# Kernel tuning notes

Hardware: AMD Instinct MI355X
Metric: run time of the kernel (lower is better)

The kernel has to match this reference:

```python
import jax, jax.numpy as jnp
import numpy as np

RADIUS = 0.1
NSAMPLE = 32
NUM_KP = 15
KP_EXTENT = 1.0
DENSITY_PARAM = 5.0
EXTENT = 2.0 * KP_EXTENT * RADIUS / DENSITY_PARAM  # 0.04
K_RADIUS = 1.5 * EXTENT                            # 0.06
C_IN, C_OUT = 64, 128
BN_EPS = 1e-5


def make_kernel_points():
    # Deterministic stand-in for create_kernel_points: first point at center
    # ('center' fixed mode), remaining points quasi-uniform in a ball of K_RADIUS.
    rs = np.random.RandomState(0)
    d = rs.randn(NUM_KP - 1, 3)
    d /= np.linalg.norm(d, axis=1, keepdims=True) + 1e-9
    r = rs.rand(NUM_KP - 1, 1) ** (1.0 / 3.0)
    pts = np.concatenate([np.zeros((1, 3)), d * r * K_RADIUS], axis=0)
    return jnp.asarray(pts, dtype=jnp.float32)  # [K, 3]


def ball_group(query_xyz, support_xyz, support_mask, radius, nsample):
    """Masked ordered ball query. Returns idx [B,N1,S] int32 and mask [B,N1,S] float."""
    # [B, N1, N2] squared distances (dominant memory traffic)
    d2 = jnp.sum((query_xyz[:, :, None, :] - support_xyz[:, None, :, :]) ** 2, axis=-1)
    valid = (d2 < radius * radius) & (support_mask[:, None, :] > 0)
    order = jnp.cumsum(valid.astype(jnp.int32), axis=-1) - 1  # rank among valid, per row
    in_cap = valid & (order < nsample)
    slot = jnp.where(in_cap, order, nsample)  # overflow -> dump slot
    B, N1, N2 = d2.shape
    j = jnp.broadcast_to(jnp.arange(N2, dtype=jnp.int32), (B, N1, N2))
    b = jnp.arange(B)[:, None, None]
    n = jnp.arange(N1)[None, :, None]
    idx = jnp.zeros((B, N1, nsample + 1), jnp.int32).at[b, n, slot].set(j)[..., :nsample]
    cnt = jnp.sum(in_cap.astype(jnp.int32), axis=-1)  # [B, N1]
    nb_mask = jnp.arange(nsample)[None, None, :] < cnt[:, :, None]
    idx = jnp.where(nb_mask, idx, idx[:, :, :1])  # pad with first neighbor
    return idx, nb_mask.astype(jnp.float32)


def setup_inputs() -> dict:
    key = jax.random.key(0)
    ks = jax.random.split(key, 6)
    B, N1, N2 = 4, 2048, 8192
    query_xyz = jax.random.uniform(ks[0], (B, N1, 3), dtype=jnp.float32)
    support_xyz = jax.random.uniform(ks[1], (B, N2, 3), dtype=jnp.float32)
    query_mask = jnp.ones((B, N1), jnp.float32)
    support_mask = jnp.ones((B, N2), jnp.float32)
    support_features = jax.random.normal(ks[2], (B, C_IN, N2), dtype=jnp.float32)
    kernel_weights = jax.random.normal(ks[3], (NUM_KP, C_IN), dtype=jnp.float32) * (1.0 / np.sqrt(C_IN))
    W_out = jax.random.normal(ks[4], (C_OUT, C_IN), dtype=jnp.float32) * (1.0 / np.sqrt(C_IN))
    gamma = jnp.ones((C_OUT,), jnp.float32)
    beta = jnp.zeros((C_OUT,), jnp.float32)
    return {
        "query_xyz": query_xyz, "support_xyz": support_xyz,
        "query_mask": query_mask, "support_mask": support_mask,
        "support_features": support_features, "K_points": make_kernel_points(),
        "kernel_weights": kernel_weights, "W_out": W_out,
        "gamma": gamma, "beta": beta,
    }


def reference(query_xyz, support_xyz, query_mask, support_mask, support_features,
              K_points, kernel_weights, W_out, gamma, beta):
    idx, nb_mask = ball_group(query_xyz, support_xyz, support_mask, RADIUS, NSAMPLE)
    # gather neighbor features: [B, N2, C] -> [B, N1, S, C]
    feats_t = jnp.transpose(support_features, (0, 2, 1))
    nbr_feats = jnp.take_along_axis(feats_t[:, None, :, :],
                                    idx[:, :, :, None], axis=2)  # [B,N1,S,C]
    # grouped relative positions: [B, N1, S, 3]
    grouped_xyz = jnp.take_along_axis(support_xyz[:, None, :, :],
                                      idx[:, :, :, None], axis=2)
    rel_pos = grouped_xyz - query_xyz[:, :, None, :]
    # kernel-point distances: [B, N1, S, K]
    diff = rel_pos[:, :, :, None, :] - K_points[None, None, None, :, :]
    sq_d = jnp.sum(diff * diff, axis=-1)
    # linear influence, then permute to [B, N1, K, S]
    w = jnp.clip(1.0 - jnp.sqrt(sq_d) / EXTENT, 0.0, None)
    w = jnp.transpose(w, (0, 1, 3, 2))
    feature_mask = nb_mask + (1.0 - query_mask[:, :, None])  # [B,N1,S]
    w = w * feature_mask[:, :, None, :]
    # weighted sum over neighbors: [B, N1, K, C]
    weighted = jnp.einsum('bnks,bnsc->bnkc', w, nbr_feats)
    out = jnp.sum(weighted * kernel_weights[None, None, :, :], axis=2)  # [B,N1,C]
    out = jnp.transpose(out, (0, 2, 1))  # [B, C_in, N1]
    # out_conv: 1x1 conv (no bias) + BatchNorm1d (training-mode batch stats) + ReLU
    out = jnp.einsum('oc,bcn->bon', W_out, out)  # [B, C_out, N1]
    mean = jnp.mean(out, axis=(0, 2), keepdims=True)
    var = jnp.mean((out - mean) ** 2, axis=(0, 2), keepdims=True)
    out = (out - mean) * jax.lax.rsqrt(var + BN_EPS)
    out = out * gamma[None, :, None] + beta[None, :, None]
    return jax.nn.relu(out)
```

## Files before the change

### kernel.cpp

```cpp
#include <hip/hip_runtime.h>
#include <stdint.h>
#include <limits.h>

#define BATCH 4
#define N1D   2048
#define N2D   8192
#define NSAMP 32
#define NKP   15
#define CIN   64
#define COUT  128

#define RAD2    0.01f
#define INV_EXT 25.0f
#define BN_EPS  1e-5f
#define CMARG   0.1000001f

#define NWAVE 4
#define QPB   NWAVE
#define NCELL 1000
#define MAXC  96

#define WS_PTS4   0
#define WS_BPTS   131072
#define WS_FEATT  262144
#define WS_OUT2   2367488
#define WS_CS     3416064
#define WS_CNT    3420160
#define WS_CUR    3424256

__device__ __forceinline__ int cell_of(float x, float y, float z) {
  int cx = (int)(x*10.f); cx = cx < 0 ? 0 : (cx > 9 ? 9 : cx);
  int cy = (int)(y*10.f); cy = cy < 0 ? 0 : (cy > 9 ? 9 : cy);
  int cz = (int)(z*10.f); cz = cz < 0 ? 0 : (cz > 9 ? 9 : cz);
  return (cx*10 + cy)*10 + cz;
}

__global__ __launch_bounds__(256) void pg_prep(
    const float* __restrict__ sxyz, const float* __restrict__ smask,
    const float* __restrict__ sfeat, float4* __restrict__ pts4,
    float* __restrict__ featT, int* __restrict__ cellCnt)
{
  __shared__ float tile[64*65];
  const int t  = threadIdx.x;
  const int bt = blockIdx.x;

  if (bt >= 512) {
    const int idx = bt - 512;
    const int bb  = idx >> 5;
    const int i   = ((idx & 31) << 8) + t;
    if (smask[bb*N2D + i] > 0.f) {
      const float* p = sxyz + ((size_t)bb*N2D + i)*3;
      atomicAdd(&cellCnt[bb*1024 + cell_of(p[0], p[1], p[2])], 1);
    }
    return;
  }

  const int b  = bt >> 7;
  const int j0 = (bt & 127) * 64;
  if (t < 64) {
    const int g = bt*64 + t;
    pts4[g] = make_float4(sxyz[g*3+0], sxyz[g*3+1], sxyz[g*3+2], 0.f);
  }
  const float* src = sfeat + (size_t)(b*CIN)*N2D + j0;
#pragma unroll
  for (int i = 0; i < 4; ++i) {
    const int c  = i*16 + (t >> 4);
    const int j4 = (t & 15) * 4;
    const float4 v = *(const float4*)(src + (size_t)c*N2D + j4);
    tile[c*65 + j4+0] = v.x;
    tile[c*65 + j4+1] = v.y;
    tile[c*65 + j4+2] = v.z;
    tile[c*65 + j4+3] = v.w;
  }
  __syncthreads();
  float* dstb = featT + (size_t)(b*N2D + j0) * CIN;
#pragma unroll
  for (int r = 0; r < 4; ++r) {
    const int j  = r*16 + (t >> 4);
    const int c4 = (t & 15) * 4;
    float4 v;
    v.x = tile[(c4+0)*65 + j];
    v.y = tile[(c4+1)*65 + j];
    v.z = tile[(c4+2)*65 + j];
    v.w = tile[(c4+3)*65 + j];
    *(float4*)(dstb + j*CIN + c4) = v;
  }
}

__global__ __launch_bounds__(256) void pg_scan(
    const int* __restrict__ cellCnt, int* __restrict__ cellStart,
    int* __restrict__ cellCur)
{
  __shared__ int off_s[NCELL+1];
  __shared__ int wsum[4];
  const int t    = threadIdx.x;
  const int lane = t & 63;
  const int wv   = t >> 6;
  const int bb   = blockIdx.x;
  const int* cnt = cellCnt + bb*1024;

  int c0 = 0, c1 = 0, c2 = 0, c3 = 0, v = 0;
  if (t < 250) {
    c0 = cnt[t*4+0]; c1 = cnt[t*4+1]; c2 = cnt[t*4+2]; c3 = cnt[t*4+3];
    v = c0 + c1 + c2 + c3;
  }
  int x = v;
#pragma unroll
  for (int off = 1; off < 64; off <<= 1) {
    int y = __shfl_up(x, off);
    if (lane >= off) x += y;
  }
  if (lane == 63) wsum[wv] = x;
  __syncthreads();
  int base = 0;
#pragma unroll
  for (int w = 0; w < 4; ++w) if (w < wv) base += wsum[w];
  const int excl = base + x - v;
  if (t < 250) {
    int o = excl;
    off_s[t*4+0] = o; o += c0;
    off_s[t*4+1] = o; o += c1;
    off_s[t*4+2] = o; o += c2;
    off_s[t*4+3] = o;
  }
  if (t == 0) off_s[NCELL] = wsum[0]+wsum[1]+wsum[2]+wsum[3];
  __syncthreads();
  for (int i = t; i < NCELL; i += 256) {
    const int o = off_s[i];
    cellStart[bb*(NCELL+1) + i] = o;
    cellCur[bb*1024 + i] = o;
  }
  if (t == 0) cellStart[bb*(NCELL+1) + NCELL] = off_s[NCELL];
}

__global__ __launch_bounds__(256) void pg_scatter(
    const float* __restrict__ sxyz, const float* __restrict__ smask,
    int* __restrict__ cellCur, float4* __restrict__ bpts)
{
  const int idx = blockIdx.x;
  const int bb  = idx >> 5;
  const int i   = ((idx & 31) << 8) + threadIdx.x;
  if (smask[bb*N2D + i] > 0.f) {
    const float* p = sxyz + ((size_t)bb*N2D + i)*3;
    const float px = p[0], py = p[1], pz = p[2];
    const int pos = atomicAdd(&cellCur[bb*1024 + cell_of(px,py,pz)], 1);
    bpts[(size_t)bb*N2D + pos] = make_float4(px, py, pz, __int_as_float(i));
  }
}

__global__ __launch_bounds__(256) void pg_main(
    const float* __restrict__ qxyz, const float* __restrict__ qmask,
    const float4* __restrict__ pts4, const float4* __restrict__ bpts,
    const int* __restrict__ cellStart, const float* __restrict__ featT,
    const float* __restrict__ Kp, const float* __restrict__ KW,
    const float* __restrict__ Wout, float* __restrict__ out2)
{
  __shared__ __align__(16) int  s_cand[QPB][MAXC];
  __shared__ int2               s_im[QPB][NSAMP];
  __shared__ float              s_w[QPB*NSAMP*17];
  __shared__ float              s_xq[QPB*68];

  const int t    = threadIdx.x;
  const int lane = t & 63;
  const int wv   = t >> 6;
  const int gbase = blockIdx.x * QPB;
  const int b     = gbase >> 11;
  const uint64_t lt = (1ull << lane) - 1ull;

  const int g = gbase + wv;
  const float qx = qxyz[g*3+0], qy = qxyz[g*3+1], qz = qxyz[g*3+2];

  const float4* bptsb = bpts + (size_t)b*N2D;
  int cq;
  {
    int cx0 = (int)((qx-CMARG)*10.f); if (cx0 < 0) cx0 = 0;
    int cx1 = (int)((qx+CMARG)*10.f); if (cx1 > 9) cx1 = 9;
    int cy0 = (int)((qy-CMARG)*10.f); if (cy0 < 0) cy0 = 0;
    int cy1 = (int)((qy+CMARG)*10.f); if (cy1 > 9) cy1 = 9;
    int cz0 = (int)((qz-CMARG)*10.f); if (cz0 < 0) cz0 = 0;
    int cz1 = (int)((qz+CMARG)*10.f); if (cz1 > 9) cz1 = 9;
    const int ny = cy1 - cy0 + 1;
    const int npair = (cx1 - cx0 + 1) * ny;

    int len = 0, rs = 0;
    if (lane < npair) {
      const int cx = cx0 + lane / ny;
      const int cy = cy0 + lane % ny;
      const int* csb = cellStart + b*(NCELL+1) + (cx*10 + cy)*10;
      rs  = csb[cz0];
      len = csb[cz1 + 1] - rs;
    }
    int pc = len;
#pragma unroll
    for (int off = 1; off < 16; off <<= 1) {
      int y = __shfl_up(pc, off);
      if (lane >= off) pc += y;
    }
    const int tot   = __shfl(pc, 15);
    const int excl  = pc - len;
    const int sbase = rs - excl;

    int segc[9], segb[9];
#pragma unroll
    for (int e = 0; e < 9; ++e) {
      const int ce = __builtin_amdgcn_readlane(excl,  e);
      const int be = __builtin_amdgcn_readlane(sbase, e);
      segc[e] = (e < npair) ? ce : INT_MAX;
      segb[e] = (e < npair) ? be : 0;
    }

    int ccnt = 0;
    for (int base0 = 0; base0 < tot; base0 += 64) {
      const int idx = base0 + lane;
      bool ok = false; int jj = 0;
      if (idx < tot) {
        int bb2 = segb[0];
#pragma unroll
        for (int e = 1; e < 9; ++e) if (segc[e] <= idx) bb2 = segb[e];
        const float4 pt = bptsb[bb2 + idx];
        const float dx = pt.x - qx, dy = pt.y - qy, dz = pt.z - qz;
        ok = (dx*dx + dy*dy + dz*dz) < RAD2;
        jj = __float_as_int(pt.w);
      }
      const uint64_t m = __ballot(ok);
      if (ok) {
        const int pos = ccnt + __popcll(m & lt);
        if (pos < MAXC) s_cand[wv][pos] = jj;
      }
      ccnt += (int)__popcll(m);
    }
    const int C = ccnt < MAXC ? ccnt : MAXC;
    const int C4 = (C + 3) & ~3;
    if (C + lane < C4) s_cand[wv][C + lane] = INT_MAX;

    int jA = (lane      < C) ? s_cand[wv][lane]      : INT_MAX;
    int jB = (lane + 64 < C) ? s_cand[wv][lane + 64] : INT_MAX;
    int rA = 0, rB = 0;
    for (int e = 0; e < C4; e += 4) {
      const int4 v4 = *(const int4*)&s_cand[wv][e];
      rA += (v4.x < jA) + (v4.y < jA) + (v4.z < jA) + (v4.w < jA);
      rB += (v4.x < jB) + (v4.y < jB) + (v4.z < jB) + (v4.w < jB);
    }
    if (lane      < C && rA < NSAMP) s_im[wv][rA].x = jA;
    if (lane + 64 < C && rB < NSAMP) s_im[wv][rB].x = jB;
    cq = C < NSAMP ? C : NSAMP;
  }

  {
    const int s    = lane & 31;
    const int half = lane >> 5;
    const int raw  = s_im[wv][s].x;
    const int r0   = s_im[wv][0].x;
    const int j = (s < cq) ? raw : (cq > 0 ? r0 : 0);
    if (half == 0) s_im[wv][s].x = j;

    const float4 pj = pts4[b*N2D + j];
    const float rx = pj.x - qx;
    const float ry = pj.y - qy;
    const float rz = pj.z - qz;

    unsigned msk = 0u;
#pragma unroll
    for (int ki = 0; ki < 8; ++ki) {
      const int k = half*8 + ki;
      if (k < NKP) {
        const float dx = rx - Kp[k*3+0];
        const float dy = ry - Kp[k*3+1];
        const float dz = rz - Kp[k*3+2];
        const float dd = dx*dx + dy*dy + dz*dz;
        const float w = 1.0f - sqrtf(dd) * INV_EXT;
        if (w > 0.0f) {
          s_w[(wv*NSAMP + s)*17 + k] = w;
          msk |= (1u << k);
        }
      }
    }
    msk |= (unsigned)__shfl_xor((int)msk, 32);
    if (half == 0) s_im[wv][s].y = (int)msk;
  }

  {
    float kw[NKP];
#pragma unroll
    for (int k = 0; k < NKP; ++k) kw[k] = KW[k*CIN + lane];

    const float fpad = 1.0f - qmask[g];
    const int cqs = __builtin_amdgcn_readfirstlane(cq);

    float ft[NSAMP];
#pragma unroll
    for (int s = 0; s < NSAMP; ++s) {
      const int j = __builtin_amdgcn_readfirstlane(s_im[wv][s].x);
      ft[s] = featT[(size_t)(b*N2D + j)*CIN + lane];
    }

    float acc = 0.0f;
#pragma unroll
    for (int s = 0; s < NSAMP; ++s) {
      const float fm = ((s < cqs) ? 1.0f : 0.0f) + fpad;
      if (fm != 0.0f) {
        const unsigned mk =
            (unsigned)__builtin_amdgcn_readfirstlane(s_im[wv][s].y);
        if (mk != 0u) {
          const float* wp = &s_w[(wv*NSAMP + s)*17];
          float wsum = 0.0f;
#pragma unroll
          for (int k = 0; k < NKP; ++k)
            if (mk & (1u << k)) wsum += wp[k] * kw[k];
          acc = fmaf(fm*wsum, ft[s], acc);
        }
      }
    }
    s_xq[wv*68 + lane] = acc;
  }
  __syncthreads();

  {
    const int n4 = t & 3;
    const int og = t >> 2;
    const int gq = gbase + n4;
    const int nn = gq & 2047;
    const float4* xr = (const float4*)&s_xq[n4*68];
    const float4* w0 = (const float4*)(Wout + (og*2+0)*CIN);
    const float4* w1 = (const float4*)(Wout + (og*2+1)*CIN);
    float a0 = 0.f, a1 = 0.f;
#pragma unroll
    for (int c4 = 0; c4 < 16; ++c4) {
      const float4 x4 = xr[c4];
      const float4 wa = w0[c4];
      const float4 wb = w1[c4];
      a0 = fmaf(wa.x, x4.x, fmaf(wa.y, x4.y, fmaf(wa.z, x4.z, fmaf(wa.w, x4.w, a0))));
      a1 = fmaf(wb.x, x4.x, fmaf(wb.y, x4.y, fmaf(wb.z, x4.z, fmaf(wb.w, x4.w, a1))));
    }
    float* ob = out2 + (size_t)(b*COUT + og*2)*N1D + nn;
    ob[0]   = a0;
    ob[N1D] = a1;
  }
}

__global__ __launch_bounds__(256) void pg_finish(
    const float* __restrict__ out2, const float* __restrict__ gamma,
    const float* __restrict__ beta, float* __restrict__ dout)
{
  __shared__ float red[8];
  __shared__ float mv[2];
  const int t  = threadIdx.x;
  const int o  = blockIdx.x & 127;
  const int bb = blockIdx.x >> 7;
  float4 f[4][2];
  float s1 = 0.f, s2 = 0.f;
#pragma unroll
  for (int r = 0; r < BATCH; ++r) {
    const float4* p = (const float4*)(out2 + (size_t)(r*COUT + o)*N1D);
#pragma unroll
    for (int i = 0; i < 2; ++i) {
      const float4 x = p[i*256 + t];
      f[r][i] = x;
      s1 += x.x + x.y + x.z + x.w;
      s2 += x.x*x.x + x.y*x.y + x.z*x.z + x.w*x.w;
    }
  }
#pragma unroll
  for (int off = 32; off; off >>= 1) {
    s1 += __shfl_xor(s1, off);
    s2 += __shfl_xor(s2, off);
  }
  const int wv = t >> 6;
  if ((t & 63) == 0) { red[wv] = s1; red[4+wv] = s2; }
  __syncthreads();
  if (t == 0) {
    const float inv = 1.0f / (float)(BATCH*N1D);
    const float mean = (red[0]+red[1]+red[2]+red[3]) * inv;
    const float var  = (red[4]+red[5]+red[6]+red[7]) * inv - mean*mean;
    mv[0] = mean;
    mv[1] = rsqrtf(var + BN_EPS);
  }
  __syncthreads();
  const float mean = mv[0];
  const float ga = gamma[o] * mv[1];
  const float be = beta[o];
  float4* dp = (float4*)(dout + (size_t)(bb*COUT + o)*N1D);
#pragma unroll
  for (int i = 0; i < 2; ++i) {
    const float4 x = f[bb][i];
    float4 y;
    y.x = fmaxf((x.x - mean)*ga + be, 0.0f);
    y.y = fmaxf((x.y - mean)*ga + be, 0.0f);
    y.z = fmaxf((x.z - mean)*ga + be, 0.0f);
    y.w = fmaxf((x.w - mean)*ga + be, 0.0f);
    dp[i*256 + t] = y;
  }
}

extern "C" void kernel_launch(void* const* d_in, const int* in_sizes, int n_in,
                              void* d_out, int out_size, void* d_ws, size_t ws_size,
                              hipStream_t stream)
{
  const float* qxyz  = (const float*)d_in[0];
  const float* sxyz  = (const float*)d_in[1];
  const float* qmask = (const float*)d_in[2];
  const float* smask = (const float*)d_in[3];
  const float* sfeat = (const float*)d_in[4];
  const float* Kp    = (const float*)d_in[5];
  const float* KW    = (const float*)d_in[6];
  const float* Wout  = (const float*)d_in[7];
  const float* gamma = (const float*)d_in[8];
  const float* beta  = (const float*)d_in[9];
  float* ws = (float*)d_ws;
  float4* pts4 = (float4*)(ws + WS_PTS4);
  float4* bpts = (float4*)(ws + WS_BPTS);
  float* featT = ws + WS_FEATT;
  float* out2  = ws + WS_OUT2;
  int*   cellS = (int*)(ws + WS_CS);
  int*   cellC = (int*)(ws + WS_CNT);
  int*   cellU = (int*)(ws + WS_CUR);
  float* dst   = (float*)d_out;

  hipMemsetAsync(cellC, 0, BATCH*1024*sizeof(int), stream);
  pg_prep   <<<640,  256, 0, stream>>>(sxyz, smask, sfeat, pts4, featT, cellC);
  pg_scan   <<<4,    256, 0, stream>>>(cellC, cellS, cellU);
  pg_scatter<<<128,  256, 0, stream>>>(sxyz, smask, cellU, bpts);
  pg_main   <<<2048, 256, 0, stream>>>(qxyz, qmask, pts4, bpts, cellS, featT,
                                       Kp, KW, Wout, out2);
  pg_finish <<<512,  256, 0, stream>>>(out2, gamma, beta, dst);
}
```

Measured before the change: 132.3 us.

## Fuse cell scan into scatter, carry candidate coords in LDS, prune far cell columns

Merges the prefix-scan and scatter kernels into one launch: every block recomputes the cell offsets and uses an atomic counter relative to the offset. The pts4 buffer goes away, since selected neighbours keep their coordinates from the binned candidates held in LDS. The change also skips cell columns whose xy distance already exceeds the radius, batches the candidate loads four at a time, and trims MAXC and the s_w stride. The cost is redundant scan work in each block and a tighter candidate cap, which risks truncation if more than 80 candidates fall inside the radius.

```diff
diff --git a/kernel.cpp b/kernel.cpp
--- a/kernel.cpp
+++ b/kernel.cpp
@@ -18,9 +18,9 @@
 #define NWAVE 4
 #define QPB   NWAVE
 #define NCELL 1000
-#define MAXC  96
-
-#define WS_PTS4   0
+#define MAXC  80
+#define NPF   4
+
 #define WS_BPTS   131072
 #define WS_FEATT  262144
 #define WS_OUT2   2367488
@@ -37,8 +37,8 @@
 
 __global__ __launch_bounds__(256) void pg_prep(
     const float* __restrict__ sxyz, const float* __restrict__ smask,
-    const float* __restrict__ sfeat, float4* __restrict__ pts4,
-    float* __restrict__ featT, int* __restrict__ cellCnt)
+    const float* __restrict__ sfeat, float* __restrict__ featT,
+    int* __restrict__ cellCnt)
 {
   __shared__ float tile[64*65];
   const int t  = threadIdx.x;
@@ -57,10 +57,6 @@
 
   const int b  = bt >> 7;
   const int j0 = (bt & 127) * 64;
-  if (t < 64) {
-    const int g = bt*64 + t;
-    pts4[g] = make_float4(sxyz[g*3+0], sxyz[g*3+1], sxyz[g*3+2], 0.f);
-  }
   const float* src = sfeat + (size_t)(b*CIN)*N2D + j0;
 #pragma unroll
   for (int i = 0; i < 4; ++i) {
@@ -87,17 +83,19 @@
   }
 }
 
-__global__ __launch_bounds__(256) void pg_scan(
-    const int* __restrict__ cellCnt, int* __restrict__ cellStart,
-    int* __restrict__ cellCur)
+__global__ __launch_bounds__(256) void pg_binscan(
+    const int* __restrict__ cellCnt, const float* __restrict__ sxyz,
+    const float* __restrict__ smask, int* __restrict__ cellCur,
+    float4* __restrict__ bpts, int* __restrict__ cellStart)
 {
   __shared__ int off_s[NCELL+1];
   __shared__ int wsum[4];
-  const int t    = threadIdx.x;
-  const int lane = t & 63;
-  const int wv   = t >> 6;
-  const int bb   = blockIdx.x;
-  const int* cnt = cellCnt + bb*1024;
+  const int t     = threadIdx.x;
+  const int lane  = t & 63;
+  const int wv    = t >> 6;
+  const int bb    = blockIdx.x >> 5;
+  const int slice = blockIdx.x & 31;
+  const int* cnt  = cellCnt + bb*1024;
 
   int c0 = 0, c1 = 0, c2 = 0, c3 = 0, v = 0;
   if (t < 250) {
@@ -125,40 +123,35 @@
   }
   if (t == 0) off_s[NCELL] = wsum[0]+wsum[1]+wsum[2]+wsum[3];
   __syncthreads();
-  for (int i = t; i < NCELL; i += 256) {
-    const int o = off_s[i];
-    cellStart[bb*(NCELL+1) + i] = o;
-    cellCur[bb*1024 + i] = o;
-  }
-  if (t == 0) cellStart[bb*(NCELL+1) + NCELL] = off_s[NCELL];
-}
-
-__global__ __launch_bounds__(256) void pg_scatter(
-    const float* __restrict__ sxyz, const float* __restrict__ smask,
-    int* __restrict__ cellCur, float4* __restrict__ bpts)
-{
-  const int idx = blockIdx.x;
-  const int bb  = idx >> 5;
-  const int i   = ((idx & 31) << 8) + threadIdx.x;
+
+  if (slice == 0) {
+    for (int i = t; i < NCELL+1; i += 256)
+      cellStart[bb*(NCELL+1) + i] = off_s[i];
+  }
+
+  const int i = slice*256 + t;
   if (smask[bb*N2D + i] > 0.f) {
     const float* p = sxyz + ((size_t)bb*N2D + i)*3;
     const float px = p[0], py = p[1], pz = p[2];
-    const int pos = atomicAdd(&cellCur[bb*1024 + cell_of(px,py,pz)], 1);
+    const int cell = cell_of(px, py, pz);
+    const int pos = off_s[cell] + atomicAdd(&cellCur[bb*1024 + cell], 1);
     bpts[(size_t)bb*N2D + pos] = make_float4(px, py, pz, __int_as_float(i));
   }
 }
 
 __global__ __launch_bounds__(256) void pg_main(
     const float* __restrict__ qxyz, const float* __restrict__ qmask,
-    const float4* __restrict__ pts4, const float4* __restrict__ bpts,
-    const int* __restrict__ cellStart, const float* __restrict__ featT,
-    const float* __restrict__ Kp, const float* __restrict__ KW,
-    const float* __restrict__ Wout, float* __restrict__ out2)
+    const float4* __restrict__ bpts, const int* __restrict__ cellStart,
+    const float* __restrict__ featT, const float* __restrict__ Kp,
+    const float* __restrict__ KW, const float* __restrict__ Wout,
+    const float* __restrict__ sxyz, float* __restrict__ out2)
 {
-  __shared__ __align__(16) int  s_cand[QPB][MAXC];
-  __shared__ int2               s_im[QPB][NSAMP];
-  __shared__ float              s_w[QPB*NSAMP*17];
-  __shared__ float              s_xq[QPB*68];
+  __shared__ __align__(16) float4 s_cand4[QPB][MAXC];
+  __shared__ __align__(16) int    s_candj[QPB][MAXC];
+  __shared__ __align__(16) float4 s_sel[QPB][NSAMP];
+  __shared__ int2                 s_jm[QPB][NSAMP];
+  __shared__ float                s_w[QPB*NSAMP*16];
+  __shared__ float                s_xq[QPB*68];
 
   const int t    = threadIdx.x;
   const int lane = t & 63;
@@ -186,9 +179,14 @@
     if (lane < npair) {
       const int cx = cx0 + lane / ny;
       const int cy = cy0 + lane % ny;
-      const int* csb = cellStart + b*(NCELL+1) + (cx*10 + cy)*10;
-      rs  = csb[cz0];
-      len = csb[cz1 + 1] - rs;
+      const float lox = cx*0.1f, loy = cy*0.1f;
+      const float dxc = fmaxf(fmaxf(lox - qx, qx - (lox+0.1f)), 0.f);
+      const float dyc = fmaxf(fmaxf(loy - qy, qy - (loy+0.1f)), 0.f);
+      if (dxc*dxc + dyc*dyc < RAD2) {
+        const int* csb = cellStart + b*(NCELL+1) + (cx*10 + cy)*10;
+        rs  = csb[cz0];
+        len = csb[cz1 + 1] - rs;
+      }
     }
     int pc = len;
 #pragma unroll
@@ -210,54 +208,68 @@
     }
 
     int ccnt = 0;
-    for (int base0 = 0; base0 < tot; base0 += 64) {
-      const int idx = base0 + lane;
-      bool ok = false; int jj = 0;
-      if (idx < tot) {
-        int bb2 = segb[0];
-#pragma unroll
-        for (int e = 1; e < 9; ++e) if (segc[e] <= idx) bb2 = segb[e];
-        const float4 pt = bptsb[bb2 + idx];
-        const float dx = pt.x - qx, dy = pt.y - qy, dz = pt.z - qz;
-        ok = (dx*dx + dy*dy + dz*dz) < RAD2;
-        jj = __float_as_int(pt.w);
+    for (int base0 = 0; base0 < tot; base0 += 64*NPF) {
+      float4 pt[NPF];
+#pragma unroll
+      for (int u = 0; u < NPF; ++u) {
+        const int idx = base0 + u*64 + lane;
+        if (idx < tot) {
+          int bb2 = segb[0];
+#pragma unroll
+          for (int e = 1; e < 9; ++e) if (segc[e] <= idx) bb2 = segb[e];
+          pt[u] = bptsb[bb2 + idx];
+        }
       }
-      const uint64_t m = __ballot(ok);
-      if (ok) {
-        const int pos = ccnt + __popcll(m & lt);
-        if (pos < MAXC) s_cand[wv][pos] = jj;
+#pragma unroll
+      for (int u = 0; u < NPF; ++u) {
+        const int idx = base0 + u*64 + lane;
+        bool ok = false;
+        if (idx < tot) {
+          const float dx = pt[u].x - qx, dy = pt[u].y - qy, dz = pt[u].z - qz;
+          ok = (dx*dx + dy*dy + dz*dz) < RAD2;
+        }
+        const uint64_t m = __ballot(ok);
+        if (ok) {
+          const int pos = ccnt + __popcll(m & lt);
+          if (pos < MAXC) {
+            s_cand4[wv][pos] = pt[u];
+            s_candj[wv][pos] = __float_as_int(pt[u].w);
+          }
+        }
+        ccnt += (int)__popcll(m);
       }
-      ccnt += (int)__popcll(m);
     }
     const int C = ccnt < MAXC ? ccnt : MAXC;
     const int C4 = (C + 3) & ~3;
-    if (C + lane < C4) s_cand[wv][C + lane] = INT_MAX;
-
-    int jA = (lane      < C) ? s_cand[wv][lane]      : INT_MAX;
-    int jB = (lane + 64 < C) ? s_cand[wv][lane + 64] : INT_MAX;
+    if (C + lane < C4) s_candj[wv][C + lane] = INT_MAX;
+
+    const int jA = (lane      < C) ? s_candj[wv][lane]      : INT_MAX;
+    const int jB = (lane + 64 < C) ? s_candj[wv][lane + 64] : INT_MAX;
     int rA = 0, rB = 0;
     for (int e = 0; e < C4; e += 4) {
-      const int4 v4 = *(const int4*)&s_cand[wv][e];
+      const int4 v4 = *(const int4*)&s_candj[wv][e];
       rA += (v4.x < jA) + (v4.y < jA) + (v4.z < jA) + (v4.w < jA);
       rB += (v4.x < jB) + (v4.y < jB) + (v4.z < jB) + (v4.w < jB);
     }
-    if (lane      < C && rA < NSAMP) s_im[wv][rA].x = jA;
-    if (lane + 64 < C && rB < NSAMP) s_im[wv][rB].x = jB;
+    if (lane      < C && rA < NSAMP) s_sel[wv][rA] = s_cand4[wv][lane];
+    if (lane + 64 < C && rB < NSAMP) s_sel[wv][rB] = s_cand4[wv][lane + 64];
     cq = C < NSAMP ? C : NSAMP;
   }
 
   {
     const int s    = lane & 31;
     const int half = lane >> 5;
-    const int raw  = s_im[wv][s].x;
-    const int r0   = s_im[wv][0].x;
-    const int j = (s < cq) ? raw : (cq > 0 ? r0 : 0);
-    if (half == 0) s_im[wv][s].x = j;
-
-    const float4 pj = pts4[b*N2D + j];
-    const float rx = pj.x - qx;
-    const float ry = pj.y - qy;
-    const float rz = pj.z - qz;
+    float4 sel;
+    if (cq > 0) {
+      sel = s_sel[wv][s < cq ? s : 0];
+    } else {
+      sel = make_float4(sxyz[(size_t)b*N2D*3+0], sxyz[(size_t)b*N2D*3+1],
+                        sxyz[(size_t)b*N2D*3+2], __int_as_float(0));
+    }
+    const int j = __float_as_int(sel.w);
+    const float rx = sel.x - qx;
+    const float ry = sel.y - qy;
+    const float rz = sel.z - qz;
 
     unsigned msk = 0u;
 #pragma unroll
@@ -270,13 +282,13 @@
         const float dd = dx*dx + dy*dy + dz*dz;
         const float w = 1.0f - sqrtf(dd) * INV_EXT;
         if (w > 0.0f) {
-          s_w[(wv*NSAMP + s)*17 + k] = w;
+          s_w[(wv*NSAMP + s)*16 + k] = w;
           msk |= (1u << k);
         }
       }
     }
     msk |= (unsigned)__shfl_xor((int)msk, 32);
-    if (half == 0) s_im[wv][s].y = (int)msk;
+    if (half == 0) s_jm[wv][s] = make_int2(j, (int)msk);
   }
 
   {
@@ -290,7 +302,7 @@
     float ft[NSAMP];
 #pragma unroll
     for (int s = 0; s < NSAMP; ++s) {
-      const int j = __builtin_amdgcn_readfirstlane(s_im[wv][s].x);
+      const int j = __builtin_amdgcn_readfirstlane(s_jm[wv][s].x);
       ft[s] = featT[(size_t)(b*N2D + j)*CIN + lane];
     }
 
@@ -300,9 +312,9 @@
       const float fm = ((s < cqs) ? 1.0f : 0.0f) + fpad;
       if (fm != 0.0f) {
         const unsigned mk =
-            (unsigned)__builtin_amdgcn_readfirstlane(s_im[wv][s].y);
+            (unsigned)__builtin_amdgcn_readfirstlane(s_jm[wv][s].y);
         if (mk != 0u) {
-          const float* wp = &s_w[(wv*NSAMP + s)*17];
+          const float* wp = &s_w[(wv*NSAMP + s)*16];
           float wsum = 0.0f;
 #pragma unroll
           for (int k = 0; k < NKP; ++k)
@@ -407,7 +419,6 @@
   const float* gamma = (const float*)d_in[8];
   const float* beta  = (const float*)d_in[9];
   float* ws = (float*)d_ws;
-  float4* pts4 = (float4*)(ws + WS_PTS4);
   float4* bpts = (float4*)(ws + WS_BPTS);
   float* featT = ws + WS_FEATT;
   float* out2  = ws + WS_OUT2;
@@ -416,11 +427,10 @@
   int*   cellU = (int*)(ws + WS_CUR);
   float* dst   = (float*)d_out;
 
-  hipMemsetAsync(cellC, 0, BATCH*1024*sizeof(int), stream);
-  pg_prep   <<<640,  256, 0, stream>>>(sxyz, smask, sfeat, pts4, featT, cellC);
-  pg_scan   <<<4,    256, 0, stream>>>(cellC, cellS, cellU);
-  pg_scatter<<<128,  256, 0, stream>>>(sxyz, smask, cellU, bpts);
-  pg_main   <<<2048, 256, 0, stream>>>(qxyz, qmask, pts4, bpts, cellS, featT,
-                                       Kp, KW, Wout, out2);
+  hipMemsetAsync(cellC, 0, 2*BATCH*1024*sizeof(int), stream);
+  pg_prep   <<<640,  256, 0, stream>>>(sxyz, smask, sfeat, featT, cellC);
+  pg_binscan<<<128,  256, 0, stream>>>(cellC, sxyz, smask, cellU, bpts, cellS);
+  pg_main   <<<2048, 256, 0, stream>>>(qxyz, qmask, bpts, cellS, featT,
+                                       Kp, KW, Wout, sxyz, out2);
   pg_finish <<<512,  256, 0, stream>>>(out2, gamma, beta, dst);
 }
```

New measurement: 132.7 us. No clear change (+0.3%).
